# Performance work log

Hardware: AMD Instinct MI355X
Metric: run time of the kernel (lower is better)

Reference implementation:

```python
import jax, jax.numpy as jnp
from jax import lax
import numpy as np

H, B, T, E, D, A, C = 4, 32, 1500, 512, 512, 256, 10
KS = 100          # conv_kernel_size
KW = 2 * KS + 1   # filter width = 201
O = 512           # att_odim
SCALING = 2.0


def setup_inputs() -> dict:
    key = jax.random.key(0)
    ks = jax.random.split(key, 12)
    s = 0.05  # param scale to keep tanh in linear-ish regime
    att_prev = jax.random.uniform(ks[3], (H, B, T), dtype=jnp.float32)
    att_prev = att_prev / jnp.sum(att_prev, axis=-1, keepdims=True)  # distribution-like
    return {
        "enc_pad": jax.random.normal(ks[0], (B, T, E), dtype=jnp.float32),
        "enc_len": jnp.full((B,), T, dtype=jnp.int32),
        "dec_z": jax.random.normal(ks[1], (B, D), dtype=jnp.float32),
        "att_prev": att_prev,
        "W_enc": jax.random.normal(ks[4], (H, E, A), dtype=jnp.float32) * s,
        "b_enc": jnp.zeros((H, A), dtype=jnp.float32),
        "W_dec": jax.random.normal(ks[5], (H, D, A), dtype=jnp.float32) * s,
        "W_att": jax.random.normal(ks[6], (H, C, A), dtype=jnp.float32) * s,
        "conv_w": jax.random.normal(ks[7], (H, C, KW), dtype=jnp.float32) * s,
        "gvec_w": jax.random.normal(ks[8], (H, A), dtype=jnp.float32) * s,
        "W_o": jax.random.normal(ks[9], (H * E, O), dtype=jnp.float32) * s,
        "b_o": jnp.zeros((O,), dtype=jnp.float32),
    }


def _loc_conv(att_prev, conv_w):
    # att_prev: [H,B,T], conv_w: [H,C,KW] -> [H,B,C,T]
    def one_head(a, k):  # a [B,T], k [C,KW]
        return lax.conv_general_dilated(
            a[:, None, :], k[:, None, :], (1,), [(KS, KS)],
            dimension_numbers=("NCH", "OIH", "NCH"))  # [B,C,T]
    return jax.vmap(one_head)(att_prev, conv_w)


def reference(enc_pad, enc_len, dec_z, att_prev, W_enc, b_enc, W_dec, W_att,
              conv_w, gvec_w, W_o, b_o):
    # pre-computed encoder projections per head: [H,B,T,A]
    pre_enc = jnp.einsum("bte,hea->hbta", enc_pad, W_enc) + b_enc[:, None, None, :]
    # decoder projection: [H,B,1,A]
    dec_proj = jnp.einsum("bd,hda->hba", dec_z, W_dec)[:, :, None, :]
    # location conv + projection: [H,B,T,A]
    conv_out = _loc_conv(att_prev, conv_w)                       # [H,B,C,T]
    att_conv = jnp.einsum("hbct,hca->hbta", conv_out, W_att)
    # additive scoring: e [H,B,T]
    att_state = jnp.tanh(pre_enc + dec_proj + att_conv)
    e = jnp.einsum("hbta,ha->hbt", att_state, gvec_w)
    w = jax.nn.softmax(SCALING * e, axis=-1)                     # [H,B,T]
    # per-head context: [H,B,E]
    c_heads = jnp.einsum("hbt,bte->hbe", w, enc_pad)
    # concat heads -> [B, H*E], then output projection
    c_cat = jnp.transpose(c_heads, (1, 0, 2)).reshape(B, H * E)
    c = c_cat @ W_o + b_o                                        # [B,O]
    return c, w
```

## Files before the change

kernel.cpp:

```cpp
#include <hip/hip_runtime.h>
#include <hip/hip_bf16.h>

#define NH 4
#define NB 32
#define NT 1500
#define NE 512
#define ND 512
#define NA 256
#define NC 10
#define NKS 100
#define NKW 201
#define NO 512
#define NBT (NB*NT)
#define RB 375
#define OSPLIT 16

typedef unsigned short u16;
typedef unsigned int u32;
typedef __attribute__((ext_vector_type(8))) short short8;
typedef __attribute__((ext_vector_type(4))) float f32x4;

__device__ __forceinline__ u16 f2bf(float f) {
  u32 x = __builtin_bit_cast(u32, f);
  return (u16)((x + 0x7FFFu + ((x >> 16) & 1u)) >> 16);
}

__device__ __forceinline__ float bf2f(u16 b) {
  return __builtin_bit_cast(float, (u32)b << 16);
}

__device__ __forceinline__ void gld_lds16(const void* g, void* l) {
  __builtin_amdgcn_global_load_lds((const __attribute__((address_space(1))) u32*)g,
                                   (__attribute__((address_space(3))) u32*)l, 16, 0, 0);
}

__device__ __forceinline__ float fast_tanh(float x) {
  float t, r;
  asm("v_exp_f32 %0, %1" : "=v"(t) : "v"(x * 2.885390082f));
  asm("v_rcp_f32 %0, %1" : "=v"(r) : "v"(t + 1.0f));
  return __builtin_fmaf(-2.0f, r, 1.0f);
}

__global__ __launch_bounds__(256) void k_prep_enc(const float* __restrict__ in,
                                                  u16* __restrict__ encp) {
  const int bx = blockIdx.x;
  const int rowblk = bx >> 3;
  const int ks = bx & 7;
  const int t = threadIdx.x;
  const int r = t >> 1;
  const int part = t & 1;
  __shared__ u16 tile[8192];

  const float* src = in + ((size_t)(rowblk * 128 + r)) * NE + ks * 64 + part * 32;
#pragma unroll
  for (int i = 0; i < 8; ++i) {
    float4 v = ((const float4*)src)[i];
    int kc = part * 4 + (i >> 1);
    int j0 = (i & 1) * 4;
    u16* d = &tile[(kc * 128 + r) * 8 + j0];
    d[0] = f2bf(v.x); d[1] = f2bf(v.y); d[2] = f2bf(v.z); d[3] = f2bf(v.w);
  }
  __syncthreads();
  u16* ob = encp + ((size_t)rowblk * 64 + ks * 8) * 1024;
  const uint4* s4 = (const uint4*)&tile[t * 32];
  uint4* d4 = (uint4*)&ob[t * 32];
  d4[0] = s4[0]; d4[1] = s4[1]; d4[2] = s4[2]; d4[3] = s4[3];
}

__global__ __launch_bounds__(256) void k_prep_w(const float* __restrict__ We,
                                                const float* __restrict__ Wa,
                                                u16* __restrict__ wc) {
  int idx = blockIdx.x * 256 + threadIdx.x;
  int h = idx / 139264;
  int r = idx % 139264;
  int kc = r / 2048; r %= 2048;
  int n = r / 8;
  int j = r % 8;
  int k = kc * 8 + j;
  float v = 0.f;
  if (k < NE) v = We[((size_t)h * NE + k) * NA + n];
  else if (k - NE < NC) v = Wa[((size_t)h * NC + (k - NE)) * NA + n];
  wc[idx] = f2bf(v);
}

__global__ __launch_bounds__(192) void k_conv(const float* __restrict__ att,
                                              const float* __restrict__ cw,
                                              u16* __restrict__ cvb) {
  int hb = blockIdx.x;
  int h = hb >> 5, b = hb & 31;
  int chunk = blockIdx.y;
  int tid = threadIdx.x;
  __shared__ float al[NT];
  __shared__ float klT[NKW * 16];
  for (int i = tid; i < NT; i += 192) al[i] = att[(size_t)hb * NT + i];
  for (int i = tid; i < NC * NKW; i += 192)
    klT[(i % NKW) * 16 + (i / NKW)] = cw[h * NC * NKW + i];
  __syncthreads();
  int start = chunk * 188;
  int len = min(188, NT - start);
  if (tid < len) {
    int t = start + tid;
    float acc[NC];
#pragma unroll
    for (int c = 0; c < NC; ++c) acc[c] = 0.f;
    int kmin = max(0, NKS - t);
    int kmax = min(NKW - 1, NT - 1 + NKS - t);
    for (int k = kmin; k <= kmax; ++k) {
      float a = al[t + k - NKS];
      float4 w0 = *(const float4*)&klT[k * 16];
      float4 w1 = *(const float4*)&klT[k * 16 + 4];
      float2 w2 = *(const float2*)&klT[k * 16 + 8];
      acc[0] += a * w0.x; acc[1] += a * w0.y; acc[2] += a * w0.z; acc[3] += a * w0.w;
      acc[4] += a * w1.x; acc[5] += a * w1.y; acc[6] += a * w1.z; acc[7] += a * w1.w;
      acc[8] += a * w2.x; acc[9] += a * w2.y;
    }
    int row = b * NT + t;
    u16* o = cvb + ((size_t)(h * RB) + (row >> 7)) * 4096 + (row & 127) * 8;
    short8 g0, g1, gz;
#pragma unroll
    for (int c = 0; c < 8; ++c) g0[c] = (short)f2bf(acc[c]);
    g1[0] = (short)f2bf(acc[8]); g1[1] = (short)f2bf(acc[9]);
#pragma unroll
    for (int c = 2; c < 8; ++c) g1[c] = 0;
#pragma unroll
    for (int c = 0; c < 8; ++c) gz[c] = 0;
    *(short8*)&o[0]    = g0;
    *(short8*)&o[1024] = g1;
    *(short8*)&o[2048] = gz;
    *(short8*)&o[3072] = gz;
  }
}

__global__ __launch_bounds__(256) void k_dproj(const float* __restrict__ dz,
                                               const float* __restrict__ wd,
                                               const float* __restrict__ be,
                                               float* __restrict__ dp) {
  int hb = blockIdx.x; int h = hb >> 5, b = hb & 31;
  int a = threadIdx.x;
  __shared__ float z[ND];
  for (int i = a; i < ND; i += 256) z[i] = dz[b * ND + i];
  __syncthreads();
  float s = be[h * NA + a];
  for (int d = 0; d < ND; ++d) s += z[d] * wd[((size_t)h * ND + d) * NA + a];
  dp[(h * NB + b) * NA + a] = s;
}

__global__ __launch_bounds__(512) void k_gemm_e(
    const u16* __restrict__ encp, const u16* __restrict__ cvb,
    const u16* __restrict__ wcomb, const float* __restrict__ dproj,
    const float* __restrict__ gvec, float* __restrict__ ebuf) {
  const int orig = blockIdx.x;
  const int xcd = orig & 7, pos = orig >> 3;
  const int wgid = (xcd < 4 ? xcd * 188 : 752 + (xcd - 4) * 187) + pos;
  const int h = wgid & 3;
  const int rowblk = wgid >> 2;
  const int row0 = rowblk * 128;
  const int tid = threadIdx.x;
  const int lane = tid & 63;
  const int wid = tid >> 6;
  const int wm = wid >> 2;
  const int wn = wid & 3;
  const int l16 = lane & 15;
  const int lh = lane >> 4;

  __shared__ u16 Alds[3][4096];
  __shared__ u16 Blds[3][8192];
  __shared__ float dp[2][NA];
  __shared__ float gl[NA];
  __shared__ float elds[128][4];

  const int b0 = row0 / NT;
  const int bound = (b0 + 1) * NT - row0;
  const int b1 = min(b0 + 1, NB - 1);
  if (tid < NA) {
    dp[0][tid] = dproj[(h * NB + b0) * NA + tid];
    gl[tid] = gvec[h * NA + tid];
  } else {
    dp[1][tid - NA] = dproj[(h * NB + b1) * NA + (tid - NA)];
  }

  f32x4 acc[4][4] = {};

  const u16* aSrc = encp + (size_t)rowblk * 65536;
  const u16* bSrc = wcomb + (size_t)h * 139264;
  const u16* aTail = cvb + ((size_t)(h * RB) + rowblk) * 4096;

  const int arow = wm * 64 + l16;
  const int bcol = wn * 64 + l16;

#define ISSUE(is, buf) do {                                         \
    const u16* ga_ = ((is) < 16) ? (aSrc + (is) * 4096) : aTail;    \
    gld_lds16(ga_ + tid * 8, &Alds[(buf)][tid * 8]);                \
    const u16* gb_ = bSrc + (is) * 8192;                            \
    gld_lds16(gb_ + tid * 8, &Blds[(buf)][tid * 8]);                \
    gld_lds16(gb_ + 4096 + tid * 8, &Blds[(buf)][4096 + tid * 8]);  \
  } while (0)

  ISSUE(0, 0);
  ISSUE(1, 1);

  int cur = 0;
  for (int ks = 0; ks < 17; ++ks) {
    if (ks < 16) asm volatile("s_waitcnt vmcnt(3)" ::: "memory");
    else         asm volatile("s_waitcnt vmcnt(0)" ::: "memory");
    __builtin_amdgcn_s_barrier();
    __builtin_amdgcn_sched_barrier(0);
    if (ks + 2 <= 16) {
      int nbuf = (cur + 2 >= 3) ? cur - 1 : cur + 2;
      ISSUE(ks + 2, nbuf);
    }
    const u16* ap = &Alds[cur][(lh * 128 + arow) * 8];
    const u16* bp = &Blds[cur][(lh * 256 + bcol) * 8];
    short8 af[4], bf4[4];
#pragma unroll
    for (int i = 0; i < 4; ++i) af[i] = *(const short8*)&ap[i * 128];
#pragma unroll
    for (int i = 0; i < 4; ++i) bf4[i] = *(const short8*)&bp[i * 128];
    __builtin_amdgcn_s_setprio(1);
#pragma unroll
    for (int i = 0; i < 4; ++i)
#pragma unroll
      for (int j = 0; j < 4; ++j)
        acc[i][j] = __builtin_amdgcn_mfma_f32_16x16x32_bf16(af[i], bf4[j], acc[i][j], 0, 0, 0);
    __builtin_amdgcn_s_setprio(0);
    cur = (cur == 2) ? 0 : cur + 1;
  }
#undef ISSUE
  __syncthreads();

  float ep[4][4];
#pragma unroll
  for (int i = 0; i < 4; ++i)
#pragma unroll
    for (int r = 0; r < 4; ++r) ep[i][r] = 0.f;

#pragma unroll
  for (int j = 0; j < 4; ++j) {
    int col = wn * 64 + j * 16 + l16;
    float g = gl[col];
    float biasLo = dp[0][col], biasHi = dp[1][col];
#pragma unroll
    for (int i = 0; i < 4; ++i) {
#pragma unroll
      for (int r = 0; r < 4; ++r) {
        int rl = wm * 64 + i * 16 + lh * 4 + r;
        float bias = (rl >= bound) ? biasHi : biasLo;
        ep[i][r] += g * fast_tanh(acc[i][j][r] + bias);
      }
    }
  }
#pragma unroll
  for (int d = 1; d < 16; d <<= 1)
#pragma unroll
    for (int i = 0; i < 4; ++i)
#pragma unroll
      for (int r = 0; r < 4; ++r) ep[i][r] += __shfl_xor(ep[i][r], d, 64);

  if (l16 == 0) {
#pragma unroll
    for (int i = 0; i < 4; ++i)
#pragma unroll
      for (int r = 0; r < 4; ++r) elds[wm * 64 + i * 16 + lh * 4 + r][wn] = ep[i][r];
  }
  __syncthreads();
  if (tid < 128) {
    float e = elds[tid][0] + elds[tid][1] + elds[tid][2] + elds[tid][3];
    ebuf[(size_t)h * NBT + row0 + tid] = e;
  }
}

__global__ __launch_bounds__(256) void k_softmax(const float* __restrict__ ebuf,
                                                 float* __restrict__ wout) {
  int hb = blockIdx.x;
  int tid = threadIdx.x, lane = tid & 63, wid = tid >> 6;
  __shared__ float el[NT];
  __shared__ float red[4];
  float m = -1e30f;
  for (int t = tid; t < NT; t += 256) {
    float v = ebuf[(size_t)hb * NT + t];
    el[t] = v;
    m = fmaxf(m, v);
  }
#pragma unroll
  for (int d = 1; d < 64; d <<= 1) m = fmaxf(m, __shfl_xor(m, d, 64));
  if (lane == 0) red[wid] = m;
  __syncthreads();
  m = fmaxf(fmaxf(red[0], red[1]), fmaxf(red[2], red[3]));
  __syncthreads();
  float s = 0.f;
  for (int t = tid; t < NT; t += 256) s += expf(2.f * (el[t] - m));
#pragma unroll
  for (int d = 1; d < 64; d <<= 1) s += __shfl_xor(s, d, 64);
  if (lane == 0) red[wid] = s;
  __syncthreads();
  s = red[0] + red[1] + red[2] + red[3];
  float inv = 1.f / s;
  for (int t = tid; t < NT; t += 256)
    wout[(size_t)hb * NT + t] = expf(2.f * (el[t] - m)) * inv;
}

__global__ __launch_bounds__(512) void k_context(const u16* __restrict__ encp,
                                                 const float* __restrict__ w,
                                                 float* __restrict__ part) {
  int b = blockIdx.x, ch = blockIdx.y;
  int tid = threadIdx.x;
  int g = tid >> 6;
  int lane = tid & 63;
  int c0 = ch * 188;
  int n = min(188, NT - c0);
  __shared__ float wl[NH][192];
  for (int i = tid; i < NH * 188; i += 512) {
    int hh = i / 188, tt = i % 188;
    wl[hh][tt] = (tt < n) ? w[((size_t)hh * NB + b) * NT + c0 + tt] : 0.f;
  }
  __syncthreads();
  float acc[NH][8];
#pragma unroll
  for (int hh = 0; hh < NH; ++hh)
#pragma unroll
    for (int j = 0; j < 8; ++j) acc[hh][j] = 0.f;

  for (int tt = g; tt < n; tt += 8) {
    int row = b * NT + c0 + tt;
    const u16* src = encp + ((size_t)(row >> 7)) * 65536 + lane * 1024 + (row & 127) * 8;
    short8 v = *(const short8*)src;
    float f[8];
#pragma unroll
    for (int j = 0; j < 8; ++j) f[j] = bf2f((u16)v[j]);
#pragma unroll
    for (int hh = 0; hh < NH; ++hh) {
      float ww = wl[hh][tt];
#pragma unroll
      for (int j = 0; j < 8; ++j) acc[hh][j] += ww * f[j];
    }
  }
  __shared__ float red[8][NE];
#pragma unroll
  for (int hh = 0; hh < NH; ++hh) {
    __syncthreads();
#pragma unroll
    for (int j = 0; j < 8; ++j) red[g][lane * 8 + j] = acc[hh][j];
    __syncthreads();
    float s = red[0][tid] + red[1][tid] + red[2][tid] + red[3][tid]
            + red[4][tid] + red[5][tid] + red[6][tid] + red[7][tid];
    part[((size_t)(ch * NH + hh) * NB + b) * NE + tid] = s;
  }
}

__global__ __launch_bounds__(512) void k_out_part(const float* __restrict__ part,
                                                  const float* __restrict__ Wo,
                                                  float* __restrict__ pout) {
  int b = blockIdx.x, is = blockIdx.y;
  int tid = threadIdx.x;
  int i0 = is * 128;
  __shared__ float cc[128];
  if (tid < 128) {
    int i = i0 + tid;
    int hh = i >> 9, ee = i & 511;
    float s = 0.f;
#pragma unroll
    for (int ch = 0; ch < 8; ++ch)
      s += part[((size_t)(ch * NH + hh) * NB + b) * NE + ee];
    cc[tid] = s;
  }
  __syncthreads();
  float acc = 0.f;
  const float* wp = Wo + (size_t)i0 * NO + tid;
#pragma unroll 4
  for (int il = 0; il < 128; il += 4) {
    float4 v = *(const float4*)&cc[il];
    acc += v.x * wp[(size_t)(il + 0) * NO];
    acc += v.y * wp[(size_t)(il + 1) * NO];
    acc += v.z * wp[(size_t)(il + 2) * NO];
    acc += v.w * wp[(size_t)(il + 3) * NO];
  }
  pout[((size_t)is * NB + b) * NO + tid] = acc;
}

__global__ __launch_bounds__(512) void k_out_red(const float* __restrict__ pout,
                                                 const float* __restrict__ bo,
                                                 float* __restrict__ cout) {
  int b = blockIdx.x, tid = threadIdx.x;
  float acc = bo[tid];
#pragma unroll
  for (int is = 0; is < OSPLIT; ++is)
    acc += pout[((size_t)is * NB + b) * NO + tid];
  cout[(size_t)b * NO + tid] = acc;
}

extern "C" void kernel_launch(void* const* d_in, const int* in_sizes, int n_in,
                              void* d_out, int out_size, void* d_ws, size_t ws_size,
                              hipStream_t stream) {
  const float* enc      = (const float*)d_in[0];
  const float* dec_z    = (const float*)d_in[2];
  const float* att_prev = (const float*)d_in[3];
  const float* W_enc    = (const float*)d_in[4];
  const float* b_enc    = (const float*)d_in[5];
  const float* W_dec    = (const float*)d_in[6];
  const float* W_att    = (const float*)d_in[7];
  const float* conv_w   = (const float*)d_in[8];
  const float* gvec_w   = (const float*)d_in[9];
  const float* W_o      = (const float*)d_in[10];
  const float* b_o      = (const float*)d_in[11];
  float* cout = (float*)d_out;
  float* wout = (float*)d_out + NB * NO;

  char* ws = (char*)d_ws;
  size_t off = 0;
  u16* encp   = (u16*)(ws + off); off += (size_t)NBT * NE * 2;
  u16* cvb    = (u16*)(ws + off); off += (size_t)NH * RB * 4096 * 2;
  u16* wcomb  = (u16*)(ws + off); off += (size_t)NH * 139264 * 2;
  float* dproj = (float*)(ws + off); off += (size_t)NH * NB * NA * 4;
  float* ebuf  = (float*)(ws + off); off += (size_t)NH * NB * NT * 4;
  float* part  = (float*)(ws + off); off += (size_t)8 * NH * NB * NE * 4;
  float* pout  = (float*)(ws + off); off += (size_t)OSPLIT * NB * NO * 4;

  hipLaunchKernelGGL(k_prep_enc, dim3(RB * 8), dim3(256), 0, stream, enc, encp);
  hipLaunchKernelGGL(k_prep_w, dim3(2176), dim3(256), 0, stream, W_enc, W_att, wcomb);
  hipLaunchKernelGGL(k_conv, dim3(128, 8), dim3(192), 0, stream, att_prev, conv_w, cvb);
  hipLaunchKernelGGL(k_dproj, dim3(128), dim3(256), 0, stream, dec_z, W_dec, b_enc, dproj);
  hipLaunchKernelGGL(k_gemm_e, dim3(1500), dim3(512), 0, stream,
                     encp, cvb, wcomb, dproj, gvec_w, ebuf);
  hipLaunchKernelGGL(k_softmax, dim3(128), dim3(256), 0, stream, ebuf, wout);
  hipLaunchKernelGGL(k_context, dim3(32, 8), dim3(512), 0, stream, encp, wout, part);
  hipLaunchKernelGGL(k_out_part, dim3(NB, OSPLIT), dim3(512), 0, stream, part, W_o, pout);
  hipLaunchKernelGGL(k_out_red, dim3(NB), dim3(512), 0, stream, pout, b_o, cout);
}
```

Measured before the change: 164.2 us.

## Merge prep kernels into one launch and fuse softmax into context kernel

Folds the four preprocessing kernels (encoder bf16 pack, weight pack, location conv, decoder projection) into a single block-range-dispatched kernel. The decoder projection is split four ways over D, and the GEMM kernel sums the four partials when it loads them. The separate softmax kernel is removed: each context block reloads all four heads' scores for its batch and recomputes max and sum before writing its slice of weights. This cuts launch count and serialization gaps, but the softmax reductions are now repeated in every chunk block and the prep kernel's shared memory footprint grows to the largest branch.

```diff
diff --git a/kernel.cpp b/kernel.cpp
--- a/kernel.cpp
+++ b/kernel.cpp
@@ -15,6 +15,12 @@
 #define RB 375
 #define OSPLIT 16
 
+#define PE_BLKS 3000
+#define PW_BLKS 2176
+#define CV_BLKS 1024
+#define DP_BLKS 512
+#define PREP_BLKS (PE_BLKS + PW_BLKS + CV_BLKS + DP_BLKS)
+
 typedef unsigned short u16;
 typedef unsigned int u32;
 typedef __attribute__((ext_vector_type(8))) short short8;
@@ -41,113 +47,110 @@
   return __builtin_fmaf(-2.0f, r, 1.0f);
 }
 
-__global__ __launch_bounds__(256) void k_prep_enc(const float* __restrict__ in,
-                                                  u16* __restrict__ encp) {
-  const int bx = blockIdx.x;
-  const int rowblk = bx >> 3;
-  const int ks = bx & 7;
-  const int t = threadIdx.x;
-  const int r = t >> 1;
-  const int part = t & 1;
-  __shared__ u16 tile[8192];
-
-  const float* src = in + ((size_t)(rowblk * 128 + r)) * NE + ks * 64 + part * 32;
-#pragma unroll
-  for (int i = 0; i < 8; ++i) {
-    float4 v = ((const float4*)src)[i];
-    int kc = part * 4 + (i >> 1);
-    int j0 = (i & 1) * 4;
-    u16* d = &tile[(kc * 128 + r) * 8 + j0];
-    d[0] = f2bf(v.x); d[1] = f2bf(v.y); d[2] = f2bf(v.z); d[3] = f2bf(v.w);
-  }
-  __syncthreads();
-  u16* ob = encp + ((size_t)rowblk * 64 + ks * 8) * 1024;
-  const uint4* s4 = (const uint4*)&tile[t * 32];
-  uint4* d4 = (uint4*)&ob[t * 32];
-  d4[0] = s4[0]; d4[1] = s4[1]; d4[2] = s4[2]; d4[3] = s4[3];
-}
-
-__global__ __launch_bounds__(256) void k_prep_w(const float* __restrict__ We,
-                                                const float* __restrict__ Wa,
-                                                u16* __restrict__ wc) {
-  int idx = blockIdx.x * 256 + threadIdx.x;
-  int h = idx / 139264;
-  int r = idx % 139264;
-  int kc = r / 2048; r %= 2048;
-  int n = r / 8;
-  int j = r % 8;
-  int k = kc * 8 + j;
-  float v = 0.f;
-  if (k < NE) v = We[((size_t)h * NE + k) * NA + n];
-  else if (k - NE < NC) v = Wa[((size_t)h * NC + (k - NE)) * NA + n];
-  wc[idx] = f2bf(v);
-}
-
-__global__ __launch_bounds__(192) void k_conv(const float* __restrict__ att,
-                                              const float* __restrict__ cw,
-                                              u16* __restrict__ cvb) {
-  int hb = blockIdx.x;
-  int h = hb >> 5, b = hb & 31;
-  int chunk = blockIdx.y;
-  int tid = threadIdx.x;
-  __shared__ float al[NT];
-  __shared__ float klT[NKW * 16];
-  for (int i = tid; i < NT; i += 192) al[i] = att[(size_t)hb * NT + i];
-  for (int i = tid; i < NC * NKW; i += 192)
-    klT[(i % NKW) * 16 + (i / NKW)] = cw[h * NC * NKW + i];
-  __syncthreads();
-  int start = chunk * 188;
-  int len = min(188, NT - start);
-  if (tid < len) {
-    int t = start + tid;
-    float acc[NC];
-#pragma unroll
-    for (int c = 0; c < NC; ++c) acc[c] = 0.f;
-    int kmin = max(0, NKS - t);
-    int kmax = min(NKW - 1, NT - 1 + NKS - t);
-    for (int k = kmin; k <= kmax; ++k) {
-      float a = al[t + k - NKS];
-      float4 w0 = *(const float4*)&klT[k * 16];
-      float4 w1 = *(const float4*)&klT[k * 16 + 4];
-      float2 w2 = *(const float2*)&klT[k * 16 + 8];
-      acc[0] += a * w0.x; acc[1] += a * w0.y; acc[2] += a * w0.z; acc[3] += a * w0.w;
-      acc[4] += a * w1.x; acc[5] += a * w1.y; acc[6] += a * w1.z; acc[7] += a * w1.w;
-      acc[8] += a * w2.x; acc[9] += a * w2.y;
-    }
-    int row = b * NT + t;
-    u16* o = cvb + ((size_t)(h * RB) + (row >> 7)) * 4096 + (row & 127) * 8;
-    short8 g0, g1, gz;
-#pragma unroll
-    for (int c = 0; c < 8; ++c) g0[c] = (short)f2bf(acc[c]);
-    g1[0] = (short)f2bf(acc[8]); g1[1] = (short)f2bf(acc[9]);
-#pragma unroll
-    for (int c = 2; c < 8; ++c) g1[c] = 0;
-#pragma unroll
-    for (int c = 0; c < 8; ++c) gz[c] = 0;
-    *(short8*)&o[0]    = g0;
-    *(short8*)&o[1024] = g1;
-    *(short8*)&o[2048] = gz;
-    *(short8*)&o[3072] = gz;
-  }
-}
-
-__global__ __launch_bounds__(256) void k_dproj(const float* __restrict__ dz,
-                                               const float* __restrict__ wd,
-                                               const float* __restrict__ be,
-                                               float* __restrict__ dp) {
-  int hb = blockIdx.x; int h = hb >> 5, b = hb & 31;
-  int a = threadIdx.x;
-  __shared__ float z[ND];
-  for (int i = a; i < ND; i += 256) z[i] = dz[b * ND + i];
-  __syncthreads();
-  float s = be[h * NA + a];
-  for (int d = 0; d < ND; ++d) s += z[d] * wd[((size_t)h * ND + d) * NA + a];
-  dp[(h * NB + b) * NA + a] = s;
+__global__ __launch_bounds__(256) void k_prep(
+    const float* __restrict__ in,
+    const float* __restrict__ We, const float* __restrict__ Wa,
+    const float* __restrict__ att, const float* __restrict__ cw,
+    const float* __restrict__ dz, const float* __restrict__ wd,
+    const float* __restrict__ be,
+    u16* __restrict__ encp, u16* __restrict__ wc,
+    u16* __restrict__ cvb, float* __restrict__ pdp) {
+  const int bid = blockIdx.x;
+  const int tid = threadIdx.x;
+
+  if (bid < PE_BLKS) {
+    const int rowblk = bid >> 3;
+    const int ks = bid & 7;
+    const int r = tid >> 1;
+    const int part = tid & 1;
+    __shared__ u16 tile[8192];
+    const float* src = in + ((size_t)(rowblk * 128 + r)) * NE + ks * 64 + part * 32;
+#pragma unroll
+    for (int i = 0; i < 8; ++i) {
+      float4 v = ((const float4*)src)[i];
+      int kc = part * 4 + (i >> 1);
+      int j0 = (i & 1) * 4;
+      u16* d = &tile[(kc * 128 + r) * 8 + j0];
+      d[0] = f2bf(v.x); d[1] = f2bf(v.y); d[2] = f2bf(v.z); d[3] = f2bf(v.w);
+    }
+    __syncthreads();
+    u16* ob = encp + ((size_t)rowblk * 64 + ks * 8) * 1024;
+    const uint4* s4 = (const uint4*)&tile[tid * 32];
+    uint4* d4 = (uint4*)&ob[tid * 32];
+    d4[0] = s4[0]; d4[1] = s4[1]; d4[2] = s4[2]; d4[3] = s4[3];
+  } else if (bid < PE_BLKS + PW_BLKS) {
+    int idx = (bid - PE_BLKS) * 256 + tid;
+    int h = idx / 139264;
+    int r = idx % 139264;
+    int kc = r / 2048; r %= 2048;
+    int n = r / 8;
+    int j = r % 8;
+    int k = kc * 8 + j;
+    float v = 0.f;
+    if (k < NE) v = We[((size_t)h * NE + k) * NA + n];
+    else if (k - NE < NC) v = Wa[((size_t)h * NC + (k - NE)) * NA + n];
+    wc[idx] = f2bf(v);
+  } else if (bid < PE_BLKS + PW_BLKS + CV_BLKS) {
+    int id = bid - (PE_BLKS + PW_BLKS);
+    int hb = id >> 3;
+    int h = hb >> 5, b = hb & 31;
+    int chunk = id & 7;
+    __shared__ float al[NT];
+    __shared__ float klT[NKW * 16];
+    for (int i = tid; i < NT; i += 256) al[i] = att[(size_t)hb * NT + i];
+    for (int i = tid; i < NC * NKW; i += 256)
+      klT[(i % NKW) * 16 + (i / NKW)] = cw[h * NC * NKW + i];
+    __syncthreads();
+    int start = chunk * 188;
+    int len = min(188, NT - start);
+    if (tid < len) {
+      int t = start + tid;
+      float acc[NC];
+#pragma unroll
+      for (int c = 0; c < NC; ++c) acc[c] = 0.f;
+      int kmin = max(0, NKS - t);
+      int kmax = min(NKW - 1, NT - 1 + NKS - t);
+      for (int k = kmin; k <= kmax; ++k) {
+        float a = al[t + k - NKS];
+        float4 w0 = *(const float4*)&klT[k * 16];
+        float4 w1 = *(const float4*)&klT[k * 16 + 4];
+        float2 w2 = *(const float2*)&klT[k * 16 + 8];
+        acc[0] += a * w0.x; acc[1] += a * w0.y; acc[2] += a * w0.z; acc[3] += a * w0.w;
+        acc[4] += a * w1.x; acc[5] += a * w1.y; acc[6] += a * w1.z; acc[7] += a * w1.w;
+        acc[8] += a * w2.x; acc[9] += a * w2.y;
+      }
+      int row = b * NT + t;
+      u16* o = cvb + ((size_t)(h * RB) + (row >> 7)) * 4096 + (row & 127) * 8;
+      short8 g0, g1, gz;
+#pragma unroll
+      for (int c = 0; c < 8; ++c) g0[c] = (short)f2bf(acc[c]);
+      g1[0] = (short)f2bf(acc[8]); g1[1] = (short)f2bf(acc[9]);
+#pragma unroll
+      for (int c = 2; c < 8; ++c) g1[c] = 0;
+#pragma unroll
+      for (int c = 0; c < 8; ++c) gz[c] = 0;
+      *(short8*)&o[0]    = g0;
+      *(short8*)&o[1024] = g1;
+      *(short8*)&o[2048] = gz;
+      *(short8*)&o[3072] = gz;
+    }
+  } else {
+    int id = bid - (PE_BLKS + PW_BLKS + CV_BLKS);
+    int hb = id >> 2, dc = id & 3;
+    int h = hb >> 5, b = hb & 31;
+    __shared__ float z[128];
+    if (tid < 128) z[tid] = dz[b * ND + dc * 128 + tid];
+    __syncthreads();
+    float s = (dc == 0) ? be[h * NA + tid] : 0.f;
+    const float* wp = wd + ((size_t)h * ND + dc * 128) * NA + tid;
+    for (int d = 0; d < 128; ++d) s += z[d] * wp[(size_t)d * NA];
+    pdp[(((size_t)dc * NH + h) * NB + b) * NA + tid] = s;
+  }
 }
 
 __global__ __launch_bounds__(512) void k_gemm_e(
     const u16* __restrict__ encp, const u16* __restrict__ cvb,
-    const u16* __restrict__ wcomb, const float* __restrict__ dproj,
+    const u16* __restrict__ wcomb, const float* __restrict__ pdp,
     const float* __restrict__ gvec, float* __restrict__ ebuf) {
   const int orig = blockIdx.x;
   const int xcd = orig & 7, pos = orig >> 3;
@@ -173,10 +176,19 @@
   const int bound = (b0 + 1) * NT - row0;
   const int b1 = min(b0 + 1, NB - 1);
   if (tid < NA) {
-    dp[0][tid] = dproj[(h * NB + b0) * NA + tid];
+    float s = 0.f;
+#pragma unroll
+    for (int dc = 0; dc < 4; ++dc)
+      s += pdp[(((size_t)dc * NH + h) * NB + b0) * NA + tid];
+    dp[0][tid] = s;
     gl[tid] = gvec[h * NA + tid];
   } else {
-    dp[1][tid - NA] = dproj[(h * NB + b1) * NA + (tid - NA)];
+    int a = tid - NA;
+    float s = 0.f;
+#pragma unroll
+    for (int dc = 0; dc < 4; ++dc)
+      s += pdp[(((size_t)dc * NH + h) * NB + b1) * NA + a];
+    dp[1][a] = s;
   }
 
   f32x4 acc[4][4] = {};
@@ -269,51 +281,75 @@
   }
 }
 
-__global__ __launch_bounds__(256) void k_softmax(const float* __restrict__ ebuf,
-                                                 float* __restrict__ wout) {
-  int hb = blockIdx.x;
-  int tid = threadIdx.x, lane = tid & 63, wid = tid >> 6;
-  __shared__ float el[NT];
-  __shared__ float red[4];
-  float m = -1e30f;
-  for (int t = tid; t < NT; t += 256) {
-    float v = ebuf[(size_t)hb * NT + t];
-    el[t] = v;
-    m = fmaxf(m, v);
-  }
-#pragma unroll
-  for (int d = 1; d < 64; d <<= 1) m = fmaxf(m, __shfl_xor(m, d, 64));
-  if (lane == 0) red[wid] = m;
-  __syncthreads();
-  m = fmaxf(fmaxf(red[0], red[1]), fmaxf(red[2], red[3]));
-  __syncthreads();
-  float s = 0.f;
-  for (int t = tid; t < NT; t += 256) s += expf(2.f * (el[t] - m));
-#pragma unroll
-  for (int d = 1; d < 64; d <<= 1) s += __shfl_xor(s, d, 64);
-  if (lane == 0) red[wid] = s;
-  __syncthreads();
-  s = red[0] + red[1] + red[2] + red[3];
-  float inv = 1.f / s;
-  for (int t = tid; t < NT; t += 256)
-    wout[(size_t)hb * NT + t] = expf(2.f * (el[t] - m)) * inv;
-}
-
 __global__ __launch_bounds__(512) void k_context(const u16* __restrict__ encp,
-                                                 const float* __restrict__ w,
+                                                 const float* __restrict__ ebuf,
+                                                 float* __restrict__ wout,
                                                  float* __restrict__ part) {
   int b = blockIdx.x, ch = blockIdx.y;
   int tid = threadIdx.x;
   int g = tid >> 6;
   int lane = tid & 63;
+  __shared__ float el[NH][NT];
+  __shared__ float wl[NH][192];
+  __shared__ float redw[NH][8];
+
+#pragma unroll
+  for (int hh = 0; hh < NH; ++hh)
+    for (int t = tid; t < NT; t += 512)
+      el[hh][t] = ebuf[((size_t)hh * NB + b) * NT + t];
+  __syncthreads();
+
+  float mx[NH];
+#pragma unroll
+  for (int hh = 0; hh < NH; ++hh) {
+    float m = -1e30f;
+    for (int t = tid; t < NT; t += 512) m = fmaxf(m, el[hh][t]);
+#pragma unroll
+    for (int d = 1; d < 64; d <<= 1) m = fmaxf(m, __shfl_xor(m, d, 64));
+    if (lane == 0) redw[hh][g] = m;
+  }
+  __syncthreads();
+#pragma unroll
+  for (int hh = 0; hh < NH; ++hh) {
+    float m = redw[hh][0];
+#pragma unroll
+    for (int i = 1; i < 8; ++i) m = fmaxf(m, redw[hh][i]);
+    mx[hh] = m;
+  }
+  __syncthreads();
+  float inv[NH];
+#pragma unroll
+  for (int hh = 0; hh < NH; ++hh) {
+    float s = 0.f;
+    for (int t = tid; t < NT; t += 512) s += expf(2.f * (el[hh][t] - mx[hh]));
+#pragma unroll
+    for (int d = 1; d < 64; d <<= 1) s += __shfl_xor(s, d, 64);
+    if (lane == 0) redw[hh][g] = s;
+  }
+  __syncthreads();
+#pragma unroll
+  for (int hh = 0; hh < NH; ++hh) {
+    float s = redw[hh][0];
+#pragma unroll
+    for (int i = 1; i < 8; ++i) s += redw[hh][i];
+    inv[hh] = 1.f / s;
+  }
+
   int c0 = ch * 188;
   int n = min(188, NT - c0);
-  __shared__ float wl[NH][192];
-  for (int i = tid; i < NH * 188; i += 512) {
-    int hh = i / 188, tt = i % 188;
-    wl[hh][tt] = (tt < n) ? w[((size_t)hh * NB + b) * NT + c0 + tt] : 0.f;
-  }
-  __syncthreads();
+#pragma unroll
+  for (int hh = 0; hh < NH; ++hh) {
+    for (int tt = tid; tt < 188; tt += 512) {
+      float w = 0.f;
+      if (tt < n) {
+        w = expf(2.f * (el[hh][c0 + tt] - mx[hh])) * inv[hh];
+        wout[((size_t)hh * NB + b) * NT + c0 + tt] = w;
+      }
+      wl[hh][tt] = w;
+    }
+  }
+  __syncthreads();
+
   float acc[NH][8];
 #pragma unroll
   for (int hh = 0; hh < NH; ++hh)
@@ -410,19 +446,18 @@
   u16* encp   = (u16*)(ws + off); off += (size_t)NBT * NE * 2;
   u16* cvb    = (u16*)(ws + off); off += (size_t)NH * RB * 4096 * 2;
   u16* wcomb  = (u16*)(ws + off); off += (size_t)NH * 139264 * 2;
-  float* dproj = (float*)(ws + off); off += (size_t)NH * NB * NA * 4;
+  float* pdp   = (float*)(ws + off); off += (size_t)4 * NH * NB * NA * 4;
   float* ebuf  = (float*)(ws + off); off += (size_t)NH * NB * NT * 4;
   float* part  = (float*)(ws + off); off += (size_t)8 * NH * NB * NE * 4;
   float* pout  = (float*)(ws + off); off += (size_t)OSPLIT * NB * NO * 4;
 
-  hipLaunchKernelGGL(k_prep_enc, dim3(RB * 8), dim3(256), 0, stream, enc, encp);
-  hipLaunchKernelGGL(k_prep_w, dim3(2176), dim3(256), 0, stream, W_enc, W_att, wcomb);
-  hipLaunchKernelGGL(k_conv, dim3(128, 8), dim3(192), 0, stream, att_prev, conv_w, cvb);
-  hipLaunchKernelGGL(k_dproj, dim3(128), dim3(256), 0, stream, dec_z, W_dec, b_enc, dproj);
+  hipLaunchKernelGGL(k_prep, dim3(PREP_BLKS), dim3(256), 0, stream,
+                     enc, W_enc, W_att, att_prev, conv_w, dec_z, W_dec, b_enc,
+                     encp, wcomb, cvb, pdp);
   hipLaunchKernelGGL(k_gemm_e, dim3(1500), dim3(512), 0, stream,
-                     encp, cvb, wcomb, dproj, gvec_w, ebuf);
-  hipLaunchKernelGGL(k_softmax, dim3(128), dim3(256), 0, stream, ebuf, wout);
-  hipLaunchKernelGGL(k_context, dim3(32, 8), dim3(512), 0, stream, encp, wout, part);
+                     encp, cvb, wcomb, pdp, gvec_w, ebuf);
+  hipLaunchKernelGGL(k_context, dim3(32, 8), dim3(512), 0, stream,
+                     encp, ebuf, wout, part);
   hipLaunchKernelGGL(k_out_part, dim3(NB, OSPLIT), dim3(512), 0, stream, part, W_o, pout);
   hipLaunchKernelGGL(k_out_red, dim3(NB), dim3(512), 0, stream, pout, b_o, cout);
 }
```

Measured after the change: 157.7 us. -4.0%, faster.
